# Kernel optimization log

Hardware: AMD Instinct MI355X
Metric: run time of the kernel (lower is better)

The kernel has to match this reference:

```python
import jax, jax.numpy as jnp
import numpy as np

NR, NA = 2, 1                 # num_raw, num_angle
QDIM = NR + 2 * NA            # 4: [r, x1=cos(th), x2=sin(th)]
DQ = NR + NA                  # 3: [dr, dth]
D = 2 * NR + 3 * NA           # 7: full state dim
HID = 256
EPS = 1e-6


def setup_inputs() -> dict:
    key = jax.random.key(0)
    ks = jax.random.split(key, 4)
    B = 32768
    x = jax.random.normal(ks[0], (B, D), dtype=jnp.float32)
    W0 = jax.random.normal(ks[1], (HID, D), dtype=jnp.float32) / np.sqrt(D)
    b0 = jnp.zeros((HID,), dtype=jnp.float32)
    W1 = jax.random.normal(ks[2], (HID, HID), dtype=jnp.float32) / np.sqrt(HID)
    b1 = jnp.zeros((HID,), dtype=jnp.float32)
    W2 = jax.random.normal(ks[3], (1, HID), dtype=jnp.float32) / np.sqrt(HID)
    b2 = jnp.zeros((1,), dtype=jnp.float32)
    return {"x": x, "W0": W0, "b0": b0, "W1": W1, "b1": b1, "W2": W2, "b2": b2}


def _lnn_forward(x, W0, b0, W1, b1, W2, b2):
    def L_single(xi):  # scalar Lagrangian of one state (D,)
        h = jnp.tanh(W0 @ xi + b0)
        h = jnp.tanh(W1 @ h + b1)
        return (W2 @ h + b2)[0]

    grad_single = jax.grad(L_single)
    gradL = jax.vmap(grad_single)(x)                       # (B, D)

    # Rows of the Hessian corresponding to d/d(dr,dth): (B, DQ, D).
    # Replaces the torch per-row autograd.grad loop with one batched jacfwd.
    def g(xi):
        return grad_single(xi)[QDIM:]                      # dL/d(dr,dth), (DQ,)
    Hrows = jax.vmap(jax.jacfwd(g))(x)                     # (B, DQ, D)

    x1 = x[:, NR:NR + NA]                                  # cos part (B, NA)
    x2 = x[:, NR + NA:QDIM]                                # sin part (B, NA)

    Jr = Hrows[:, :, :NR]                                  # (B, DQ, NR)
    Jx1 = Hrows[:, :, NR:NR + NA]                          # (B, DQ, NA)
    Jx2 = Hrows[:, :, NR + NA:QDIM]                        # (B, DQ, NA)
    Hdq = Hrows[:, :, QDIM:] + EPS * jnp.eye(DQ, dtype=x.dtype)  # (B, DQ, DQ)

    # chain rule back to angle theta: d/dth = -x2 * d/dx1 + x1 * d/dx2
    Jth = -x2[:, None, :] * Jx1 + x1[:, None, :] * Jx2     # (B, DQ, NA)
    Jrth = jnp.concatenate([Jr, Jth], axis=2)              # (B, DQ, DQ)

    dLdr = gradL[:, :NR]
    dLdx1 = gradL[:, NR:NR + NA]
    dLdx2 = gradL[:, NR + NA:QDIM]
    dLdth = -x2 * dLdx1 + x1 * dLdx2
    dLdrdth = jnp.concatenate([dLdr, dLdth], axis=1)       # (B, DQ)

    dq = x[:, QDIM:]                                       # (B, DQ)
    dq_term = jnp.einsum('bij,bj->bi', Jrth, dq)

    rhs = dLdrdth - dq_term                                # control = 0 (no controlNet)
    ddq = jnp.linalg.solve(Hdq, rhs[..., None])[..., 0]    # (B, DQ)

    dr = dq[:, :NR]
    dth = dq[:, NR:]
    dx1 = -x2 * dth
    dx2 = x1 * dth
    return jnp.concatenate([dr, dx1, dx2, ddq], axis=1)    # (B, D)


def reference(x, W0, b0, W1, b1, W2, b2):
    return _lnn_forward(x, W0, b0, W1, b1, W2, b2)
```

## Files before the change

### kernel.cpp

```cpp
#include <hip/hip_runtime.h>
#include <math.h>

#define HID 256
#define EPS_REG 1e-6

typedef __attribute__((ext_vector_type(8))) short short8;
typedef __attribute__((ext_vector_type(4))) short short4v;
typedef __attribute__((ext_vector_type(4))) float v4f;

#define MFMA_BF16(a, b, c) __builtin_amdgcn_mfma_f32_16x16x32_bf16((a), (b), (c), 0, 0, 0)

__device__ __forceinline__ float fast_tanh(float z) {
    const float e = __expf(2.0f * z);
    const float d = e + 1.0f;
    float r = __builtin_amdgcn_rcpf(d);
    r = r * (2.0f - d * r);
    return fmaf(-2.0f, r, 1.0f);
}

__device__ __forceinline__ float rtn_bf16(float v, short* s) {
    unsigned r = (__float_as_uint(v) + 0x8000u) & 0xFFFF0000u;
    *s = (short)(r >> 16);
    return __uint_as_float(r);
}
__device__ __forceinline__ void split3(float v, short* a, short* b, short* c) {
    float f0 = rtn_bf16(v, a);
    float r1 = v - f0;
    float f1 = rtn_bf16(r1, b);
    float r2 = r1 - f1;
    (void)rtn_bf16(r2, c);
}

__global__ void prep_w1_frags(const float* __restrict__ W1, short* __restrict__ ws) {
    const int gid   = blockIdx.x * 128 + threadIdx.x;
    const int lane  = gid & 63;
    const int ks    = (gid >> 6) & 7;
    const int rt    = (gid >> 9) & 15;
    const int which = gid >> 13;
    const int m = lane & 15, q = lane >> 4;

    float v[8];
    if (which == 0) {
        const float* p = W1 + (size_t)(rt*16 + m)*HID + ks*32 + q*8;
        const float4 va = *(const float4*)(p);
        const float4 vb = *(const float4*)(p + 4);
        v[0]=va.x; v[1]=va.y; v[2]=va.z; v[3]=va.w;
        v[4]=vb.x; v[5]=vb.y; v[6]=vb.z; v[7]=vb.w;
    } else {
        const float* p = W1 + (size_t)(ks*32 + q*8)*HID + rt*16 + m;
#pragma unroll
        for (int t = 0; t < 8; ++t) v[t] = p[(size_t)t*HID];
    }
    short8 h8, m8, l8;
#pragma unroll
    for (int t = 0; t < 8; ++t) {
        short sh, sm, sl;
        split3(v[t], &sh, &sm, &sl);
        h8[t] = sh; m8[t] = sm; l8[t] = sl;
    }
    const size_t base = (size_t)which*3*65536 + ((size_t)(rt*8 + ks)*64 + lane)*8;
    *(short8*)(ws + base)          = h8;
    *(short8*)(ws + base + 65536)  = m8;
    *(short8*)(ws + base + 131072) = l8;
}

#define FRAG_NT_STRIDE 13056
#define FRAG_BUF_STRIDE 4352

__device__ __forceinline__ void lnn_phase0(const float* __restrict__ x,
    const float* __restrict__ W0, const float* __restrict__ b0,
    int samp_base, short* __restrict__ Bf, float* __restrict__ M0, int tid)
{
    const int jq = tid & 63;
    const int s  = tid >> 6;
    const int j0 = jq * 4;
    const float* xs = x + (size_t)(samp_base + s)*7;
    float xv[7];
#pragma unroll
    for (int d = 0; d < 7; ++d) xv[d] = xs[d];
    float4 wv[7];
    const float* wp = W0 + (size_t)j0*7;
#pragma unroll
    for (int k = 0; k < 7; ++k) wv[k] = *(const float4*)(wp + 4*k);
    const float* wf = (const float*)wv;
    const int nt = s >> 2;
    const int cb = (s & 3) * 4;
    const int G  = j0 >> 3;
    const int t0 = j0 & 7;
    short4v hi4[4], mi4[4], lo4[4];
#pragma unroll
    for (int jj = 0; jj < 4; ++jj) {
        const int j = j0 + jj;
        float z = b0[j];
#pragma unroll
        for (int d = 0; d < 7; ++d) z = fmaf(wf[jj*7 + d], xv[d], z);
        const float h  = fast_tanh(z);
        const float sg = 1.0f - h*h;
        M0[j*9 + s] = h;
        float vals[4] = {h, sg*wf[jj*7 + 4], sg*wf[jj*7 + 5], sg*wf[jj*7 + 6]};
#pragma unroll
        for (int comp = 0; comp < 4; ++comp) {
            short sh, sm, sl;
            split3(vals[comp], &sh, &sm, &sl);
            hi4[comp][jj] = sh; mi4[comp][jj] = sm; lo4[comp][jj] = sl;
        }
    }
#pragma unroll
    for (int comp = 0; comp < 4; ++comp) {
        const int a = nt*FRAG_NT_STRIDE + G*136 + t0 + (cb + comp)*8;
        *(short4v*)(&Bf[a])                     = hi4[comp];
        *(short4v*)(&Bf[a + FRAG_BUF_STRIDE])   = mi4[comp];
        *(short4v*)(&Bf[a + 2*FRAG_BUF_STRIDE]) = lo4[comp];
    }
}

__device__ __forceinline__ void lnn_mm(const short8* __restrict__ Ah,
    const short8* __restrict__ Am, const short8* __restrict__ Al,
    const short* __restrict__ Bf, int w, int lane, int boff, v4f acc[2][2])
{
    short8 pah[2][2], pam[2][2], pal[2][2];
#pragma unroll
    for (int rtl = 0; rtl < 2; ++rtl) {
        const size_t fi = ((size_t)((w*2 + rtl)*8))*64 + lane;
        pah[0][rtl] = Ah[fi]; pam[0][rtl] = Am[fi]; pal[0][rtl] = Al[fi];
    }
#pragma unroll
    for (int ks = 0; ks < 8; ++ks) {
        const int cur = ks & 1, nxt = cur ^ 1;
        if (ks < 7) {
#pragma unroll
            for (int rtl = 0; rtl < 2; ++rtl) {
                const size_t fi = ((size_t)((w*2 + rtl)*8 + ks + 1))*64 + lane;
                pah[nxt][rtl] = Ah[fi]; pam[nxt][rtl] = Am[fi]; pal[nxt][rtl] = Al[fi];
            }
        }
        short8 bh[2], bm[2], bl[2];
#pragma unroll
        for (int nt = 0; nt < 2; ++nt) {
            const int a = nt*FRAG_NT_STRIDE + ks*544 + boff;
            bh[nt] = *(const short8*)(&Bf[a]);
            bm[nt] = *(const short8*)(&Bf[a + FRAG_BUF_STRIDE]);
            bl[nt] = *(const short8*)(&Bf[a + 2*FRAG_BUF_STRIDE]);
        }
        const short8 ah0 = pah[cur][0], ah1 = pah[cur][1];
        const short8 am0 = pam[cur][0], am1 = pam[cur][1];
        const short8 al0 = pal[cur][0], al1 = pal[cur][1];
        acc[0][0] = MFMA_BF16(ah0, bl[0], acc[0][0]);
        acc[0][1] = MFMA_BF16(ah0, bl[1], acc[0][1]);
        acc[1][0] = MFMA_BF16(ah1, bl[0], acc[1][0]);
        acc[1][1] = MFMA_BF16(ah1, bl[1], acc[1][1]);

        acc[0][0] = MFMA_BF16(al0, bh[0], acc[0][0]);
        acc[0][1] = MFMA_BF16(al0, bh[1], acc[0][1]);
        acc[1][0] = MFMA_BF16(al1, bh[0], acc[1][0]);
        acc[1][1] = MFMA_BF16(al1, bh[1], acc[1][1]);

        acc[0][0] = MFMA_BF16(am0, bm[0], acc[0][0]);
        acc[0][1] = MFMA_BF16(am0, bm[1], acc[0][1]);
        acc[1][0] = MFMA_BF16(am1, bm[0], acc[1][0]);
        acc[1][1] = MFMA_BF16(am1, bm[1], acc[1][1]);

        acc[0][0] = MFMA_BF16(am0, bh[0], acc[0][0]);
        acc[0][1] = MFMA_BF16(am0, bh[1], acc[0][1]);
        acc[1][0] = MFMA_BF16(am1, bh[0], acc[1][0]);
        acc[1][1] = MFMA_BF16(am1, bh[1], acc[1][1]);

        acc[0][0] = MFMA_BF16(ah0, bm[0], acc[0][0]);
        acc[0][1] = MFMA_BF16(ah0, bm[1], acc[0][1]);
        acc[1][0] = MFMA_BF16(ah1, bm[0], acc[1][0]);
        acc[1][1] = MFMA_BF16(ah1, bm[1], acc[1][1]);

        acc[0][0] = MFMA_BF16(ah0, bh[0], acc[0][0]);
        acc[0][1] = MFMA_BF16(ah0, bh[1], acc[0][1]);
        acc[1][0] = MFMA_BF16(ah1, bh[0], acc[1][0]);
        acc[1][1] = MFMA_BF16(ah1, bh[1], acc[1][1]);
    }
}

__device__ __forceinline__ void lnn_epi1(v4f acc[2][2], short* __restrict__ Bf,
    const float* __restrict__ b1, const float* __restrict__ W2,
    int w, int lane, int q, int c)
{
    const int myreg = c & 3;
    const int qbase = lane & ~3;
#pragma unroll
    for (int rtl = 0; rtl < 2; ++rtl) {
        const int base = (w*2 + rtl)*16;
        float b1r[4], w2r[4];
#pragma unroll
        for (int r = 0; r < 4; ++r) {
            b1r[r] = b1[base + q*4 + r];
            w2r[r] = W2[base + q*4 + r];
        }
        const int G  = (base >> 3) + (q >> 1);
        const int tq = (q & 1) * 4;
#pragma unroll
        for (int nt = 0; nt < 2; ++nt) {
            const float zb0 = __shfl(acc[rtl][nt][0] + b1r[0], qbase, 64);
            const float zb1 = __shfl(acc[rtl][nt][1] + b1r[1], qbase, 64);
            const float zb2 = __shfl(acc[rtl][nt][2] + b1r[2], qbase, 64);
            const float zb3 = __shfl(acc[rtl][nt][3] + b1r[3], qbase, 64);
            const float zsel = (myreg == 0) ? zb0
                             : (myreg == 1) ? zb1
                             : (myreg == 2) ? zb2 : zb3;
            const float ht = fast_tanh(zsel);
            const float st = 1.0f - ht*ht;
            float h1v[4], s1v[4];
#pragma unroll
            for (int r = 0; r < 4; ++r) {
                h1v[r] = __shfl(ht, qbase + r, 64);
                s1v[r] = __shfl(st, qbase + r, 64);
            }
            short4v ph, pm, pl;
#pragma unroll
            for (int r = 0; r < 4; ++r) {
                const float av = acc[rtl][nt][r];
                const float u  = (myreg == 0) ? (w2r[r]*s1v[r])
                                              : (-2.0f*w2r[r]*h1v[r]*s1v[r])*av;
                short sh, sm, sl;
                split3(u, &sh, &sm, &sl);
                ph[r] = sh; pm[r] = sm; pl[r] = sl;
            }
            const int a = nt*FRAG_NT_STRIDE + G*136 + c*8 + tq;
            *(short4v*)(&Bf[a])                     = ph;
            *(short4v*)(&Bf[a + FRAG_BUF_STRIDE])   = pm;
            *(short4v*)(&Bf[a + 2*FRAG_BUF_STRIDE]) = pl;
        }
    }
}

__device__ __forceinline__ void lnn_epi2(v4f acc2[2][2], short* __restrict__ Bf,
    const float* __restrict__ M0, const float* __restrict__ W0,
    int w, int lane, int q, int c)
{
    float* U0 = (float*)Bf;
#pragma unroll
    for (int rtl = 0; rtl < 2; ++rtl) {
#pragma unroll
        for (int reg = 0; reg < 4; ++reg) {
            const int j = (w*2 + rtl)*16 + q*4 + reg;
            const float w0sel = W0[j*7 + 3 + (c & 3)];
#pragma unroll
            for (int nt = 0; nt < 2; ++nt) {
                const int s = nt*4 + (c >> 2);
                const float pv = acc2[rtl][nt][reg];
                const float p0 = __shfl(pv, lane & ~3, 64);
                const float h0 = M0[j*9 + s];
                const float sg = 1.0f - h0*h0;
                const float t2 = -2.0f * p0 * h0 * sg;
                const float res = ((c & 3) == 0) ? (p0*sg)
                                                 : fmaf(pv, sg, t2 * w0sel);
                U0[j*36 + s*4 + (c & 3)] = res;
            }
        }
    }
}

__device__ __forceinline__ void lnn_phase3(const float* __restrict__ x,
    const float* __restrict__ W0, short* __restrict__ Bf,
    int samp_base, float* __restrict__ out, int w, int tid)
{
    const float* U0 = (const float*)Bf;
    float* scratch = ((float*)Bf) + 9216 + w * 425;
    const int t = tid & 63;
    float part[25];
#pragma unroll
    for (int qq = 0; qq < 25; ++qq) part[qq] = 0.0f;

#pragma unroll
    for (int m = 0; m < 4; ++m) {
        const int j = t + 64*m;
        const float4 uv = *(const float4*)(&U0[j*36 + w*4]);
        float w0d[7];
#pragma unroll
        for (int d = 0; d < 7; ++d) w0d[d] = W0[j*7 + d];
#pragma unroll
        for (int d = 0; d < 4; ++d) part[d] = fmaf(uv.x, w0d[d], part[d]);
#pragma unroll
        for (int d = 0; d < 7; ++d) {
            part[4  + d] = fmaf(uv.y, w0d[d], part[4  + d]);
            part[11 + d] = fmaf(uv.z, w0d[d], part[11 + d]);
            part[18 + d] = fmaf(uv.w, w0d[d], part[18 + d]);
        }
    }
#pragma unroll
    for (int off = 1; off <= 2; off <<= 1)
#pragma unroll
        for (int qq = 0; qq < 25; ++qq)
            part[qq] += __shfl_xor(part[qq], off, 64);
    {
        const int quad = t >> 2;
        if ((t & 3) == 0) {
#pragma unroll
            for (int e = 0; e < 25; ++e)
                scratch[e*17 + quad] = part[e];
        }
    }
    if (t < 25) {
        float tot = 0.0f;
#pragma unroll
        for (int k = 0; k < 16; ++k) tot += scratch[t*17 + k];
        scratch[t*17 + 16] = tot;
    }

    if (t == 0) {
        double g[25];
#pragma unroll
        for (int e = 0; e < 25; ++e) g[e] = (double)scratch[e*17 + 16];

        const float* xs = x + (size_t)(samp_base + w)*7;
        const double x1 = xs[2], x2 = xs[3];
        const double dq0 = xs[4], dq1 = xs[5], dth = xs[6];

        double M[3][3], rhs[3];
#pragma unroll
        for (int i = 0; i < 3; ++i) {
            const double J0 = g[4 + i*7 + 0];
            const double J1 = g[4 + i*7 + 1];
            const double J2 = -x2*g[4 + i*7 + 2] + x1*g[4 + i*7 + 3];
            const double dL = (i == 0) ? g[0]
                            : (i == 1) ? g[1]
                            : (-x2*g[2] + x1*g[3]);
            M[i][0] = g[4 + i*7 + 4] + (i == 0 ? EPS_REG : 0.0);
            M[i][1] = g[4 + i*7 + 5] + (i == 1 ? EPS_REG : 0.0);
            M[i][2] = g[4 + i*7 + 6] + (i == 2 ? EPS_REG : 0.0);
            rhs[i]  = dL - (J0*dq0 + J1*dq1 + J2*dth);
        }
        const double c00 = M[1][1]*M[2][2] - M[1][2]*M[2][1];
        const double c01 = M[1][2]*M[2][0] - M[1][0]*M[2][2];
        const double c02 = M[1][0]*M[2][1] - M[1][1]*M[2][0];
        const double det = M[0][0]*c00 + M[0][1]*c01 + M[0][2]*c02;
        const double inv = 1.0 / det;
        const double c10 = M[0][2]*M[2][1] - M[0][1]*M[2][2];
        const double c11 = M[0][0]*M[2][2] - M[0][2]*M[2][0];
        const double c12 = M[0][1]*M[2][0] - M[0][0]*M[2][1];
        const double c20 = M[0][1]*M[1][2] - M[0][2]*M[1][1];
        const double c21 = M[0][2]*M[1][0] - M[0][0]*M[1][2];
        const double c22 = M[0][0]*M[1][1] - M[0][1]*M[1][0];
        const double sol0 = (c00*rhs[0] + c10*rhs[1] + c20*rhs[2]) * inv;
        const double sol1 = (c01*rhs[0] + c11*rhs[1] + c21*rhs[2]) * inv;
        const double sol2 = (c02*rhs[0] + c12*rhs[1] + c22*rhs[2]) * inv;

        float* o = out + (size_t)(samp_base + w)*7;
        o[0] = (float)dq0;
        o[1] = (float)dq1;
        o[2] = (float)(-x2*dth);
        o[3] = (float)( x1*dth);
        o[4] = (float)sol0;
        o[5] = (float)sol1;
        o[6] = (float)sol2;
    }
}

__global__ __launch_bounds__(512, 4)
void lnn_mfma(const float* __restrict__ x,
              const float* __restrict__ W0, const float* __restrict__ b0,
              const float* __restrict__ b1, const float* __restrict__ W2,
              const short* __restrict__ ws,
              float* __restrict__ out)
{
    __shared__ __align__(16) short Bfrag[26112];
    __shared__ float M0h[HID * 9];

    const int tid   = threadIdx.x;
    const int samp0 = blockIdx.x * 8;
    const int lane  = tid & 63;
    const int w     = tid >> 6;

    lnn_phase0(x, W0, b0, samp0, Bfrag, M0h, tid);
    __syncthreads();

    const short8* A1h = (const short8*)ws;
    const short8* A1m = A1h + 8192;
    const short8* A1l = A1h + 16384;
    const short8* A2h = A1h + 24576;
    const short8* A2m = A1h + 32768;
    const short8* A2l = A1h + 40960;

    const int q = lane >> 4;
    const int c = lane & 15;
    const int boff = q*136 + c*8;

    v4f acc[2][2];
#pragma unroll
    for (int r = 0; r < 2; ++r)
#pragma unroll
        for (int n = 0; n < 2; ++n) acc[r][n] = (v4f){0.f, 0.f, 0.f, 0.f};
    lnn_mm(A1h, A1m, A1l, Bfrag, w, lane, boff, acc);
    __syncthreads();

    lnn_epi1(acc, Bfrag, b1, W2, w, lane, q, c);
    __syncthreads();

    v4f acc2[2][2];
#pragma unroll
    for (int r = 0; r < 2; ++r)
#pragma unroll
        for (int n = 0; n < 2; ++n) acc2[r][n] = (v4f){0.f, 0.f, 0.f, 0.f};
    lnn_mm(A2h, A2m, A2l, Bfrag, w, lane, boff, acc2);
    __syncthreads();

    lnn_epi2(acc2, Bfrag, M0h, W0, w, lane, q, c);
    __syncthreads();

    lnn_phase3(x, W0, Bfrag, samp0, out, w, tid);
}

#define TS8 8
#define SCP 36

__global__ void transpose_w1(const float* __restrict__ W1, float* __restrict__ W1T) {
    __shared__ float tile[32][33];
    const int bx = blockIdx.x & 7;
    const int by = blockIdx.x >> 3;
    const int tx = threadIdx.x & 31;
    const int ty = threadIdx.x >> 5;
#pragma unroll
    for (int q = 0; q < 4; ++q)
        tile[ty + q*8][tx] = W1[(by*32 + ty + q*8)*HID + bx*32 + tx];
    __syncthreads();
#pragma unroll
    for (int q = 0; q < 4; ++q)
        W1T[(bx*32 + ty + q*8)*HID + by*32 + tx] = tile[tx][ty + q*8];
}

__global__ __launch_bounds__(256, 2)
void lnn_fused(const float* __restrict__ x,
               const float* __restrict__ W0, const float* __restrict__ b0,
               const float* __restrict__ W1, const float* __restrict__ b1,
               const float* __restrict__ W2,
               const float* __restrict__ W1T, const int useT,
               float* __restrict__ out)
{
    __shared__ float M0[HID * SCP];
    __shared__ float U [HID * SCP];
    const int tid   = threadIdx.x;
    const int samp0 = blockIdx.x * TS8;
    {
        const int j = tid;
        float w0r[7];
#pragma unroll
        for (int d = 0; d < 7; ++d) w0r[d] = W0[j*7 + d];
        const float bj = b0[j];
#pragma unroll
        for (int s = 0; s < TS8; ++s) {
            const float* xs = x + (size_t)(samp0 + s)*7;
            float z = bj;
#pragma unroll
            for (int d = 0; d < 7; ++d) z = fmaf(w0r[d], xs[d], z);
            const float h  = tanhf(z);
            const float sg = 1.0f - h*h;
            float4 v = {h, sg * w0r[4], sg * w0r[5], sg * w0r[6]};
            *(float4*)(&M0[j*SCP + s*4]) = v;
        }
    }
    __syncthreads();
    const int it = tid & 63;
    const int ct = tid >> 6;
    float acc[4][8];
#pragma unroll
    for (int r = 0; r < 4; ++r)
#pragma unroll
        for (int c = 0; c < 8; ++c) acc[r][c] = 0.0f;
    if (useT) {
#pragma unroll 4
        for (int j = 0; j < HID; ++j) {
            const float4 w4 = *(const float4*)(W1T + (size_t)j*HID + it*4);
            const float4 ma = *(const float4*)(&M0[j*SCP + ct*8]);
            const float4 mb = *(const float4*)(&M0[j*SCP + ct*8 + 4]);
            const float w[4] = {w4.x, w4.y, w4.z, w4.w};
            const float m[8] = {ma.x, ma.y, ma.z, ma.w, mb.x, mb.y, mb.z, mb.w};
#pragma unroll
            for (int r = 0; r < 4; ++r)
#pragma unroll
                for (int c = 0; c < 8; ++c)
                    acc[r][c] = fmaf(w[r], m[c], acc[r][c]);
        }
    } else {
#pragma unroll 2
        for (int j = 0; j < HID; ++j) {
            float w[4];
#pragma unroll
            for (int r = 0; r < 4; ++r) w[r] = W1[(size_t)(it*4 + r)*HID + j];
            const float4 ma = *(const float4*)(&M0[j*SCP + ct*8]);
            const float4 mb = *(const float4*)(&M0[j*SCP + ct*8 + 4]);
            const float m[8] = {ma.x, ma.y, ma.z, ma.w, mb.x, mb.y, mb.z, mb.w};
#pragma unroll
            for (int r = 0; r < 4; ++r)
#pragma unroll
                for (int c = 0; c < 8; ++c)
                    acc[r][c] = fmaf(w[r], m[c], acc[r][c]);
        }
    }
    {
#pragma unroll
        for (int r = 0; r < 4; ++r) {
            const int i = it*4 + r;
            const float b1i = b1[i];
            const float w2i = W2[i];
#pragma unroll
            for (int cs = 0; cs < 2; ++cs) {
                const float z1 = acc[r][cs*4+0] + b1i;
                const float h1 = tanhf(z1);
                const float s1 = 1.0f - h1*h1;
                float4 uv;
                uv.x = w2i * s1;
                const float m2 = -2.0f * w2i * h1 * s1;
                uv.y = m2 * acc[r][cs*4+1];
                uv.z = m2 * acc[r][cs*4+2];
                uv.w = m2 * acc[r][cs*4+3];
                *(float4*)(&U[i*SCP + ct*8 + cs*4]) = uv;
            }
        }
    }
    __syncthreads();
    float acc2[4][8];
#pragma unroll
    for (int r = 0; r < 4; ++r)
#pragma unroll
        for (int c = 0; c < 8; ++c) acc2[r][c] = 0.0f;
#pragma unroll 4
    for (int i = 0; i < HID; ++i) {
        const float4 w4 = *(const float4*)(W1 + (size_t)i*HID + it*4);
        const float4 ua = *(const float4*)(&U[i*SCP + ct*8]);
        const float4 ub = *(const float4*)(&U[i*SCP + ct*8 + 4]);
        const float w[4] = {w4.x, w4.y, w4.z, w4.w};
        const float m[8] = {ua.x, ua.y, ua.z, ua.w, ub.x, ub.y, ub.z, ub.w};
#pragma unroll
        for (int r = 0; r < 4; ++r)
#pragma unroll
            for (int c = 0; c < 8; ++c)
                acc2[r][c] = fmaf(w[r], m[c], acc2[r][c]);
    }
    __syncthreads();
    {
#pragma unroll
        for (int r = 0; r < 4; ++r) {
            const int j = it*4 + r;
#pragma unroll
            for (int cs = 0; cs < 2; ++cs) {
                const int scb = ct*8 + cs*4;
                const float4 mm = *(const float4*)(&M0[j*SCP + scb]);
                const float h0v = mm.x;
                const float sg  = 1.0f - h0v*h0v;
                const float p   = acc2[r][cs*4+0];
                const float t2  = -2.0f * p * h0v;
                float4 uv;
                uv.x = p * sg;
                uv.y = fmaf(acc2[r][cs*4+1], sg, t2 * mm.y);
                uv.z = fmaf(acc2[r][cs*4+2], sg, t2 * mm.z);
                uv.w = fmaf(acc2[r][cs*4+3], sg, t2 * mm.w);
                *(float4*)(&U[j*SCP + scb]) = uv;
            }
        }
    }
    __syncthreads();
    const int s = tid >> 5;
    const int t = tid & 31;
    float part[25];
#pragma unroll
    for (int qq = 0; qq < 25; ++qq) part[qq] = 0.0f;
#pragma unroll
    for (int m = 0; m < 8; ++m) {
        const int j = t + 32*m;
        const float4 uv = *(const float4*)(&U[j*SCP + s*4]);
        float w0d[7];
#pragma unroll
        for (int d = 0; d < 7; ++d) w0d[d] = W0[j*7 + d];
#pragma unroll
        for (int d = 0; d < 4; ++d) part[d] = fmaf(uv.x, w0d[d], part[d]);
#pragma unroll
        for (int d = 0; d < 7; ++d) {
            part[4  + d] = fmaf(uv.y, w0d[d], part[4  + d]);
            part[11 + d] = fmaf(uv.z, w0d[d], part[11 + d]);
            part[18 + d] = fmaf(uv.w, w0d[d], part[18 + d]);
        }
    }
#pragma unroll
    for (int off = 16; off >= 1; off >>= 1)
#pragma unroll
        for (int qq = 0; qq < 25; ++qq)
            part[qq] += __shfl_xor(part[qq], off, 64);
    if (t == 0) {
        const float* xs = x + (size_t)(samp0 + s)*7;
        const double x1 = xs[2], x2 = xs[3];
        const double dq0 = xs[4], dq1 = xs[5], dth = xs[6];
        double A[3][4];
#pragma unroll
        for (int i = 0; i < 3; ++i) {
            const double J0 = part[4 + i*7 + 0];
            const double J1 = part[4 + i*7 + 1];
            const double J2 = -x2*(double)part[4 + i*7 + 2] + x1*(double)part[4 + i*7 + 3];
            const double dL = (i == 0) ? (double)part[0]
                            : (i == 1) ? (double)part[1]
                            : (-x2*(double)part[2] + x1*(double)part[3]);
            A[i][0] = (double)part[4 + i*7 + 4] + (i == 0 ? EPS_REG : 0.0);
            A[i][1] = (double)part[4 + i*7 + 5] + (i == 1 ? EPS_REG : 0.0);
            A[i][2] = (double)part[4 + i*7 + 6] + (i == 2 ? EPS_REG : 0.0);
            A[i][3] = dL - (J0*dq0 + J1*dq1 + J2*dth);
        }
        for (int cc = 0; cc < 2; ++cc) {
            int piv = cc;
            double mx = fabs(A[cc][cc]);
            for (int rr = cc + 1; rr < 3; ++rr) {
                const double v = fabs(A[rr][cc]);
                if (v > mx) { mx = v; piv = rr; }
            }
            if (piv != cc) {
                for (int k2 = 0; k2 < 4; ++k2) {
                    const double tmp = A[cc][k2]; A[cc][k2] = A[piv][k2]; A[piv][k2] = tmp;
                }
            }
            const double inv = 1.0 / A[cc][cc];
            for (int rr = cc + 1; rr < 3; ++rr) {
                const double f = A[rr][cc] * inv;
                for (int k2 = cc + 1; k2 < 4; ++k2) A[rr][k2] -= f * A[cc][k2];
            }
        }
        const double sol2 = A[2][3] / A[2][2];
        const double sol1 = (A[1][3] - A[1][2]*sol2) / A[1][1];
        const double sol0 = (A[0][3] - A[0][1]*sol1 - A[0][2]*sol2) / A[0][0];
        float* o = out + (size_t)(samp0 + s)*7;
        o[0] = (float)dq0;
        o[1] = (float)dq1;
        o[2] = (float)(-x2*dth);
        o[3] = (float)( x1*dth);
        o[4] = (float)sol0;
        o[5] = (float)sol1;
        o[6] = (float)sol2;
    }
}

extern "C" void kernel_launch(void* const* d_in, const int* in_sizes, int n_in,
                              void* d_out, int out_size, void* d_ws, size_t ws_size,
                              hipStream_t stream) {
    const float* x  = (const float*)d_in[0];
    const float* W0 = (const float*)d_in[1];
    const float* b0 = (const float*)d_in[2];
    const float* W1 = (const float*)d_in[3];
    const float* b1 = (const float*)d_in[4];
    const float* W2 = (const float*)d_in[5];
    float* out = (float*)d_out;

    const int B = in_sizes[0] / 7;
    const size_t NEED = 6u * 65536u * sizeof(short);

    if (ws_size >= NEED && (B % 8) == 0) {
        short* ws = (short*)d_ws;
        prep_w1_frags<<<128, 128, 0, stream>>>(W1, ws);
        lnn_mfma<<<B / 8, 512, 0, stream>>>(x, W0, b0, b1, W2, ws, out);
    } else {
        const int useT = (ws_size >= (size_t)HID * HID * sizeof(float)) ? 1 : 0;
        float* W1T = (float*)d_ws;
        if (useT) transpose_w1<<<64, 256, 0, stream>>>(W1, W1T);
        lnn_fused<<<B / TS8, 256, 0, stream>>>(x, W0, b0, W1, b1, W2, W1T, useT, out);
    }
}
```

Measured before the change: 276.0 us.

## Switch W1 matmuls to 32x32x16 bf16 MFMA with re-laid-out fragments

Replaces the 16x16x32 bf16 MFMA tiling (2x2 accumulator tiles per wave) with a single 32x32x16 MFMA accumulator per wave. The W1 fragment prep, the phase-0 B-fragment construction (now using cross-lane shuffles), and both epilogues are rewritten for the new register layout. The final 3x3 solve moves to a separate step where 8 threads each handle one sample after a barrier. The intent is fewer MFMA issues and less LDS fragment traffic per K step, at the cost of more shuffles in phase 0 and an extra synchronization.

```diff
diff --git a/kernel.cpp b/kernel.cpp
--- a/kernel.cpp
+++ b/kernel.cpp
@@ -4,11 +4,11 @@
 #define HID 256
 #define EPS_REG 1e-6
 
-typedef __attribute__((ext_vector_type(8))) short short8;
-typedef __attribute__((ext_vector_type(4))) short short4v;
-typedef __attribute__((ext_vector_type(4))) float v4f;
-
-#define MFMA_BF16(a, b, c) __builtin_amdgcn_mfma_f32_16x16x32_bf16((a), (b), (c), 0, 0, 0)
+typedef __attribute__((ext_vector_type(8)))  short short8;
+typedef __attribute__((ext_vector_type(4)))  short short4v;
+typedef __attribute__((ext_vector_type(16))) float v16f;
+
+#define MFMA32(a, b, c) __builtin_amdgcn_mfma_f32_32x32x16_bf16((a), (b), (c), 0, 0, 0)
 
 __device__ __forceinline__ float fast_tanh(float z) {
     const float e = __expf(2.0f * z);
@@ -34,20 +34,21 @@
 __global__ void prep_w1_frags(const float* __restrict__ W1, short* __restrict__ ws) {
     const int gid   = blockIdx.x * 128 + threadIdx.x;
     const int lane  = gid & 63;
-    const int ks    = (gid >> 6) & 7;
-    const int rt    = (gid >> 9) & 15;
+    const int kstep = (gid >> 6) & 15;
+    const int rt    = (gid >> 10) & 7;
     const int which = gid >> 13;
-    const int m = lane & 15, q = lane >> 4;
+    const int r32   = lane & 31;
+    const int kh    = lane >> 5;
 
     float v[8];
     if (which == 0) {
-        const float* p = W1 + (size_t)(rt*16 + m)*HID + ks*32 + q*8;
+        const float* p = W1 + (size_t)(rt*32 + r32)*HID + kstep*16 + kh*8;
         const float4 va = *(const float4*)(p);
         const float4 vb = *(const float4*)(p + 4);
         v[0]=va.x; v[1]=va.y; v[2]=va.z; v[3]=va.w;
         v[4]=vb.x; v[5]=vb.y; v[6]=vb.z; v[7]=vb.w;
     } else {
-        const float* p = W1 + (size_t)(ks*32 + q*8)*HID + rt*16 + m;
+        const float* p = W1 + (size_t)(kstep*16 + kh*8)*HID + rt*32 + r32;
 #pragma unroll
         for (int t = 0; t < 8; ++t) v[t] = p[(size_t)t*HID];
     }
@@ -58,207 +59,162 @@
         split3(v[t], &sh, &sm, &sl);
         h8[t] = sh; m8[t] = sm; l8[t] = sl;
     }
-    const size_t base = (size_t)which*3*65536 + ((size_t)(rt*8 + ks)*64 + lane)*8;
+    const size_t base = (size_t)which*196608 + ((size_t)(rt*16 + kstep)*64 + lane)*8;
     *(short8*)(ws + base)          = h8;
     *(short8*)(ws + base + 65536)  = m8;
     *(short8*)(ws + base + 131072) = l8;
 }
 
-#define FRAG_NT_STRIDE 13056
-#define FRAG_BUF_STRIDE 4352
+#define SMEM_SHORTS 25248
 
 __device__ __forceinline__ void lnn_phase0(const float* __restrict__ x,
     const float* __restrict__ W0, const float* __restrict__ b0,
     int samp_base, short* __restrict__ Bf, float* __restrict__ M0, int tid)
 {
-    const int jq = tid & 63;
-    const int s  = tid >> 6;
-    const int j0 = jq * 4;
+    const int col  = tid & 31;
+    const int s    = col >> 2;
+    const int comp = col & 3;
+    const int grp  = tid >> 5;
+    const int jb   = grp * 16;
+    const int lane = tid & 63;
+
     const float* xs = x + (size_t)(samp_base + s)*7;
     float xv[7];
 #pragma unroll
     for (int d = 0; d < 7; ++d) xv[d] = xs[d];
-    float4 wv[7];
-    const float* wp = W0 + (size_t)j0*7;
-#pragma unroll
-    for (int k = 0; k < 7; ++k) wv[k] = *(const float4*)(wp + 4*k);
-    const float* wf = (const float*)wv;
-    const int nt = s >> 2;
-    const int cb = (s & 3) * 4;
-    const int G  = j0 >> 3;
-    const int t0 = j0 & 7;
-    short4v hi4[4], mi4[4], lo4[4];
+
+    float hown[4];
 #pragma unroll
     for (int jj = 0; jj < 4; ++jj) {
-        const int j = j0 + jj;
+        const int j = jb + comp*4 + jj;
         float z = b0[j];
 #pragma unroll
-        for (int d = 0; d < 7; ++d) z = fmaf(wf[jj*7 + d], xv[d], z);
-        const float h  = fast_tanh(z);
-        const float sg = 1.0f - h*h;
-        M0[j*9 + s] = h;
-        float vals[4] = {h, sg*wf[jj*7 + 4], sg*wf[jj*7 + 5], sg*wf[jj*7 + 6]};
-#pragma unroll
-        for (int comp = 0; comp < 4; ++comp) {
+        for (int d = 0; d < 7; ++d) z = fmaf(W0[j*7 + d], xv[d], z);
+        hown[jj] = fast_tanh(z);
+        M0[j*9 + s] = hown[jj];
+    }
+
+#pragma unroll
+    for (int oct = 0; oct < 2; ++oct) {
+        short8 vh, vm, vl;
+#pragma unroll
+        for (int k = 0; k < 8; ++k) {
+            const int jidx = oct*8 + k;
+            const int j = jb + jidx;
+            const int owner = (lane & ~3) | (jidx >> 2);
+            float hsrc;
+            switch (jidx & 3) {
+                case 0: hsrc = hown[0]; break;
+                case 1: hsrc = hown[1]; break;
+                case 2: hsrc = hown[2]; break;
+                default: hsrc = hown[3]; break;
+            }
+            const float h  = __shfl(hsrc, owner, 64);
+            const float sg = 1.0f - h*h;
+            const float val = (comp == 0) ? h : (sg * W0[j*7 + 3 + comp]);
             short sh, sm, sl;
-            split3(vals[comp], &sh, &sm, &sl);
-            hi4[comp][jj] = sh; mi4[comp][jj] = sm; lo4[comp][jj] = sl;
-        }
-    }
-#pragma unroll
-    for (int comp = 0; comp < 4; ++comp) {
-        const int a = nt*FRAG_NT_STRIDE + G*136 + t0 + (cb + comp)*8;
-        *(short4v*)(&Bf[a])                     = hi4[comp];
-        *(short4v*)(&Bf[a + FRAG_BUF_STRIDE])   = mi4[comp];
-        *(short4v*)(&Bf[a + 2*FRAG_BUF_STRIDE]) = lo4[comp];
-    }
-}
-
-__device__ __forceinline__ void lnn_mm(const short8* __restrict__ Ah,
+            split3(val, &sh, &sm, &sl);
+            vh[k] = sh; vm[k] = sm; vl[k] = sl;
+        }
+        const int o = grp*2 + oct;
+        const int a = (o*32 + col)*8;
+        *(short8*)(&Bf[a])         = vh;
+        *(short8*)(&Bf[a + 8192])  = vm;
+        *(short8*)(&Bf[a + 16384]) = vl;
+    }
+}
+
+__device__ __forceinline__ void lnn_mm32(const short8* __restrict__ Ah,
     const short8* __restrict__ Am, const short8* __restrict__ Al,
-    const short* __restrict__ Bf, int w, int lane, int boff, v4f acc[2][2])
-{
-    short8 pah[2][2], pam[2][2], pal[2][2];
-#pragma unroll
-    for (int rtl = 0; rtl < 2; ++rtl) {
-        const size_t fi = ((size_t)((w*2 + rtl)*8))*64 + lane;
-        pah[0][rtl] = Ah[fi]; pam[0][rtl] = Am[fi]; pal[0][rtl] = Al[fi];
-    }
-#pragma unroll
-    for (int ks = 0; ks < 8; ++ks) {
+    const short* __restrict__ Bf, int w, int lane, v16f& acc)
+{
+    short8 pah[2], pam[2], pal[2];
+    {
+        const size_t fi = ((size_t)(w*16))*64 + lane;
+        pah[0] = Ah[fi]; pam[0] = Am[fi]; pal[0] = Al[fi];
+    }
+#pragma unroll
+    for (int ks = 0; ks < 16; ++ks) {
         const int cur = ks & 1, nxt = cur ^ 1;
-        if (ks < 7) {
-#pragma unroll
-            for (int rtl = 0; rtl < 2; ++rtl) {
-                const size_t fi = ((size_t)((w*2 + rtl)*8 + ks + 1))*64 + lane;
-                pah[nxt][rtl] = Ah[fi]; pam[nxt][rtl] = Am[fi]; pal[nxt][rtl] = Al[fi];
-            }
-        }
-        short8 bh[2], bm[2], bl[2];
-#pragma unroll
-        for (int nt = 0; nt < 2; ++nt) {
-            const int a = nt*FRAG_NT_STRIDE + ks*544 + boff;
-            bh[nt] = *(const short8*)(&Bf[a]);
-            bm[nt] = *(const short8*)(&Bf[a + FRAG_BUF_STRIDE]);
-            bl[nt] = *(const short8*)(&Bf[a + 2*FRAG_BUF_STRIDE]);
-        }
-        const short8 ah0 = pah[cur][0], ah1 = pah[cur][1];
-        const short8 am0 = pam[cur][0], am1 = pam[cur][1];
-        const short8 al0 = pal[cur][0], al1 = pal[cur][1];
-        acc[0][0] = MFMA_BF16(ah0, bl[0], acc[0][0]);
-        acc[0][1] = MFMA_BF16(ah0, bl[1], acc[0][1]);
-        acc[1][0] = MFMA_BF16(ah1, bl[0], acc[1][0]);
-        acc[1][1] = MFMA_BF16(ah1, bl[1], acc[1][1]);
-
-        acc[0][0] = MFMA_BF16(al0, bh[0], acc[0][0]);
-        acc[0][1] = MFMA_BF16(al0, bh[1], acc[0][1]);
-        acc[1][0] = MFMA_BF16(al1, bh[0], acc[1][0]);
-        acc[1][1] = MFMA_BF16(al1, bh[1], acc[1][1]);
-
-        acc[0][0] = MFMA_BF16(am0, bm[0], acc[0][0]);
-        acc[0][1] = MFMA_BF16(am0, bm[1], acc[0][1]);
-        acc[1][0] = MFMA_BF16(am1, bm[0], acc[1][0]);
-        acc[1][1] = MFMA_BF16(am1, bm[1], acc[1][1]);
-
-        acc[0][0] = MFMA_BF16(am0, bh[0], acc[0][0]);
-        acc[0][1] = MFMA_BF16(am0, bh[1], acc[0][1]);
-        acc[1][0] = MFMA_BF16(am1, bh[0], acc[1][0]);
-        acc[1][1] = MFMA_BF16(am1, bh[1], acc[1][1]);
-
-        acc[0][0] = MFMA_BF16(ah0, bm[0], acc[0][0]);
-        acc[0][1] = MFMA_BF16(ah0, bm[1], acc[0][1]);
-        acc[1][0] = MFMA_BF16(ah1, bm[0], acc[1][0]);
-        acc[1][1] = MFMA_BF16(ah1, bm[1], acc[1][1]);
-
-        acc[0][0] = MFMA_BF16(ah0, bh[0], acc[0][0]);
-        acc[0][1] = MFMA_BF16(ah0, bh[1], acc[0][1]);
-        acc[1][0] = MFMA_BF16(ah1, bh[0], acc[1][0]);
-        acc[1][1] = MFMA_BF16(ah1, bh[1], acc[1][1]);
-    }
-}
-
-__device__ __forceinline__ void lnn_epi1(v4f acc[2][2], short* __restrict__ Bf,
-    const float* __restrict__ b1, const float* __restrict__ W2,
-    int w, int lane, int q, int c)
-{
-    const int myreg = c & 3;
-    const int qbase = lane & ~3;
-#pragma unroll
-    for (int rtl = 0; rtl < 2; ++rtl) {
-        const int base = (w*2 + rtl)*16;
-        float b1r[4], w2r[4];
-#pragma unroll
-        for (int r = 0; r < 4; ++r) {
-            b1r[r] = b1[base + q*4 + r];
-            w2r[r] = W2[base + q*4 + r];
-        }
-        const int G  = (base >> 3) + (q >> 1);
-        const int tq = (q & 1) * 4;
-#pragma unroll
-        for (int nt = 0; nt < 2; ++nt) {
-            const float zb0 = __shfl(acc[rtl][nt][0] + b1r[0], qbase, 64);
-            const float zb1 = __shfl(acc[rtl][nt][1] + b1r[1], qbase, 64);
-            const float zb2 = __shfl(acc[rtl][nt][2] + b1r[2], qbase, 64);
-            const float zb3 = __shfl(acc[rtl][nt][3] + b1r[3], qbase, 64);
-            const float zsel = (myreg == 0) ? zb0
-                             : (myreg == 1) ? zb1
-                             : (myreg == 2) ? zb2 : zb3;
-            const float ht = fast_tanh(zsel);
-            const float st = 1.0f - ht*ht;
-            float h1v[4], s1v[4];
-#pragma unroll
-            for (int r = 0; r < 4; ++r) {
-                h1v[r] = __shfl(ht, qbase + r, 64);
-                s1v[r] = __shfl(st, qbase + r, 64);
-            }
-            short4v ph, pm, pl;
-#pragma unroll
-            for (int r = 0; r < 4; ++r) {
-                const float av = acc[rtl][nt][r];
-                const float u  = (myreg == 0) ? (w2r[r]*s1v[r])
-                                              : (-2.0f*w2r[r]*h1v[r]*s1v[r])*av;
-                short sh, sm, sl;
-                split3(u, &sh, &sm, &sl);
-                ph[r] = sh; pm[r] = sm; pl[r] = sl;
-            }
-            const int a = nt*FRAG_NT_STRIDE + G*136 + c*8 + tq;
-            *(short4v*)(&Bf[a])                     = ph;
-            *(short4v*)(&Bf[a + FRAG_BUF_STRIDE])   = pm;
-            *(short4v*)(&Bf[a + 2*FRAG_BUF_STRIDE]) = pl;
-        }
-    }
-}
-
-__device__ __forceinline__ void lnn_epi2(v4f acc2[2][2], short* __restrict__ Bf,
-    const float* __restrict__ M0, const float* __restrict__ W0,
-    int w, int lane, int q, int c)
+        if (ks < 15) {
+            const size_t fi = ((size_t)(w*16 + ks + 1))*64 + lane;
+            pah[nxt] = Ah[fi]; pam[nxt] = Am[fi]; pal[nxt] = Al[fi];
+        }
+        const int a = (ks*64 + lane)*8;
+        const short8 bh = *(const short8*)(&Bf[a]);
+        const short8 bm = *(const short8*)(&Bf[a + 8192]);
+        const short8 bl = *(const short8*)(&Bf[a + 16384]);
+        const short8 ah = pah[cur], am = pam[cur], al = pal[cur];
+        acc = MFMA32(ah, bl, acc);
+        acc = MFMA32(al, bh, acc);
+        acc = MFMA32(am, bm, acc);
+        acc = MFMA32(am, bh, acc);
+        acc = MFMA32(ah, bm, acc);
+        acc = MFMA32(ah, bh, acc);
+    }
+}
+
+__device__ __forceinline__ void lnn_epi1_32(const v16f& acc, short* __restrict__ Bf,
+    const float* __restrict__ b1, const float* __restrict__ W2, int w, int lane)
+{
+    const int col  = lane & 31;
+    const int comp = lane & 3;
+    const int hb   = lane >> 5;
+    const int ib   = w*32 + 4*hb;
+#pragma unroll
+    for (int rg = 0; rg < 4; ++rg) {
+        short4v ph, pm, pl;
+#pragma unroll
+        for (int rr = 0; rr < 4; ++rr) {
+            const int reg = rg*4 + rr;
+            const int i = ib + 8*rg + rr;
+            const float z0 = __shfl(acc[reg] + b1[i], lane & ~3, 64);
+            const float h1 = fast_tanh(z0);
+            const float s1 = 1.0f - h1*h1;
+            const float av = acc[reg];
+            const float w2i = W2[i];
+            const float u  = (comp == 0) ? (w2i*s1)
+                                         : (-2.0f*w2i*h1*s1)*av;
+            short sh, sm, sl;
+            split3(u, &sh, &sm, &sl);
+            ph[rr] = sh; pm[rr] = sm; pl[rr] = sl;
+        }
+        const int a = (((w*2 + (rg>>1))*64) + (((rg & 1) << 5) | col))*8 + 4*hb;
+        *(short4v*)(&Bf[a])         = ph;
+        *(short4v*)(&Bf[a + 8192])  = pm;
+        *(short4v*)(&Bf[a + 16384]) = pl;
+    }
+}
+
+__device__ __forceinline__ void lnn_epi2_32(const v16f& acc2, short* __restrict__ Bf,
+    const float* __restrict__ M0, const float* __restrict__ W0, int w, int lane)
 {
     float* U0 = (float*)Bf;
-#pragma unroll
-    for (int rtl = 0; rtl < 2; ++rtl) {
-#pragma unroll
-        for (int reg = 0; reg < 4; ++reg) {
-            const int j = (w*2 + rtl)*16 + q*4 + reg;
-            const float w0sel = W0[j*7 + 3 + (c & 3)];
-#pragma unroll
-            for (int nt = 0; nt < 2; ++nt) {
-                const int s = nt*4 + (c >> 2);
-                const float pv = acc2[rtl][nt][reg];
-                const float p0 = __shfl(pv, lane & ~3, 64);
-                const float h0 = M0[j*9 + s];
-                const float sg = 1.0f - h0*h0;
-                const float t2 = -2.0f * p0 * h0 * sg;
-                const float res = ((c & 3) == 0) ? (p0*sg)
-                                                 : fmaf(pv, sg, t2 * w0sel);
-                U0[j*36 + s*4 + (c & 3)] = res;
-            }
-        }
-    }
-}
-
-__device__ __forceinline__ void lnn_phase3(const float* __restrict__ x,
-    const float* __restrict__ W0, short* __restrict__ Bf,
-    int samp_base, float* __restrict__ out, int w, int tid)
+    const int col  = lane & 31;
+    const int s    = col >> 2;
+    const int comp = lane & 3;
+    const int hb   = lane >> 5;
+#pragma unroll
+    for (int rg = 0; rg < 4; ++rg) {
+#pragma unroll
+        for (int rr = 0; rr < 4; ++rr) {
+            const int reg = rg*4 + rr;
+            const int j = w*32 + 8*rg + 4*hb + rr;
+            const float w0sel = W0[j*7 + 3 + comp];
+            const float pv = acc2[reg];
+            const float p0 = __shfl(pv, lane & ~3, 64);
+            const float h0 = M0[j*9 + s];
+            const float sg = 1.0f - h0*h0;
+            const float t2 = -2.0f * p0 * h0 * sg;
+            const float res = (comp == 0) ? (p0*sg)
+                                          : fmaf(pv, sg, t2 * w0sel);
+            U0[j*36 + col] = res;
+        }
+    }
+}
+
+__device__ __forceinline__ void lnn_phase3_sums(const float* __restrict__ W0,
+    short* __restrict__ Bf, int w, int tid)
 {
     const float* U0 = (const float*)Bf;
     float* scratch = ((float*)Bf) + 9216 + w * 425;
@@ -302,64 +258,69 @@
         for (int k = 0; k < 16; ++k) tot += scratch[t*17 + k];
         scratch[t*17 + 16] = tot;
     }
-
-    if (t == 0) {
-        double g[25];
-#pragma unroll
-        for (int e = 0; e < 25; ++e) g[e] = (double)scratch[e*17 + 16];
-
-        const float* xs = x + (size_t)(samp_base + w)*7;
-        const double x1 = xs[2], x2 = xs[3];
-        const double dq0 = xs[4], dq1 = xs[5], dth = xs[6];
-
-        double M[3][3], rhs[3];
-#pragma unroll
-        for (int i = 0; i < 3; ++i) {
-            const double J0 = g[4 + i*7 + 0];
-            const double J1 = g[4 + i*7 + 1];
-            const double J2 = -x2*g[4 + i*7 + 2] + x1*g[4 + i*7 + 3];
-            const double dL = (i == 0) ? g[0]
-                            : (i == 1) ? g[1]
-                            : (-x2*g[2] + x1*g[3]);
-            M[i][0] = g[4 + i*7 + 4] + (i == 0 ? EPS_REG : 0.0);
-            M[i][1] = g[4 + i*7 + 5] + (i == 1 ? EPS_REG : 0.0);
-            M[i][2] = g[4 + i*7 + 6] + (i == 2 ? EPS_REG : 0.0);
-            rhs[i]  = dL - (J0*dq0 + J1*dq1 + J2*dth);
-        }
-        const double c00 = M[1][1]*M[2][2] - M[1][2]*M[2][1];
-        const double c01 = M[1][2]*M[2][0] - M[1][0]*M[2][2];
-        const double c02 = M[1][0]*M[2][1] - M[1][1]*M[2][0];
-        const double det = M[0][0]*c00 + M[0][1]*c01 + M[0][2]*c02;
-        const double inv = 1.0 / det;
-        const double c10 = M[0][2]*M[2][1] - M[0][1]*M[2][2];
-        const double c11 = M[0][0]*M[2][2] - M[0][2]*M[2][0];
-        const double c12 = M[0][1]*M[2][0] - M[0][0]*M[2][1];
-        const double c20 = M[0][1]*M[1][2] - M[0][2]*M[1][1];
-        const double c21 = M[0][2]*M[1][0] - M[0][0]*M[1][2];
-        const double c22 = M[0][0]*M[1][1] - M[0][1]*M[1][0];
-        const double sol0 = (c00*rhs[0] + c10*rhs[1] + c20*rhs[2]) * inv;
-        const double sol1 = (c01*rhs[0] + c11*rhs[1] + c21*rhs[2]) * inv;
-        const double sol2 = (c02*rhs[0] + c12*rhs[1] + c22*rhs[2]) * inv;
-
-        float* o = out + (size_t)(samp_base + w)*7;
-        o[0] = (float)dq0;
-        o[1] = (float)dq1;
-        o[2] = (float)(-x2*dth);
-        o[3] = (float)( x1*dth);
-        o[4] = (float)sol0;
-        o[5] = (float)sol1;
-        o[6] = (float)sol2;
-    }
+}
+
+__device__ __forceinline__ void lnn_solve8(const float* __restrict__ x,
+    short* __restrict__ Bf, int samp_base, float* __restrict__ out, int tid)
+{
+    if (tid >= 8) return;
+    const int s = tid;
+    const float* scratch = ((const float*)Bf) + 9216 + s * 425;
+    double g[25];
+#pragma unroll
+    for (int e = 0; e < 25; ++e) g[e] = (double)scratch[e*17 + 16];
+
+    const float* xs = x + (size_t)(samp_base + s)*7;
+    const double x1 = xs[2], x2 = xs[3];
+    const double dq0 = xs[4], dq1 = xs[5], dth = xs[6];
+
+    double M[3][3], rhs[3];
+#pragma unroll
+    for (int i = 0; i < 3; ++i) {
+        const double J0 = g[4 + i*7 + 0];
+        const double J1 = g[4 + i*7 + 1];
+        const double J2 = -x2*g[4 + i*7 + 2] + x1*g[4 + i*7 + 3];
+        const double dL = (i == 0) ? g[0]
+                        : (i == 1) ? g[1]
+                        : (-x2*g[2] + x1*g[3]);
+        M[i][0] = g[4 + i*7 + 4] + (i == 0 ? EPS_REG : 0.0);
+        M[i][1] = g[4 + i*7 + 5] + (i == 1 ? EPS_REG : 0.0);
+        M[i][2] = g[4 + i*7 + 6] + (i == 2 ? EPS_REG : 0.0);
+        rhs[i]  = dL - (J0*dq0 + J1*dq1 + J2*dth);
+    }
+    const double c00 = M[1][1]*M[2][2] - M[1][2]*M[2][1];
+    const double c01 = M[1][2]*M[2][0] - M[1][0]*M[2][2];
+    const double c02 = M[1][0]*M[2][1] - M[1][1]*M[2][0];
+    const double det = M[0][0]*c00 + M[0][1]*c01 + M[0][2]*c02;
+    const double inv = 1.0 / det;
+    const double c10 = M[0][2]*M[2][1] - M[0][1]*M[2][2];
+    const double c11 = M[0][0]*M[2][2] - M[0][2]*M[2][0];
+    const double c12 = M[0][1]*M[2][0] - M[0][0]*M[2][1];
+    const double c20 = M[0][1]*M[1][2] - M[0][2]*M[1][1];
+    const double c21 = M[0][2]*M[1][0] - M[0][0]*M[1][2];
+    const double c22 = M[0][0]*M[1][1] - M[0][1]*M[1][0];
+    const double sol0 = (c00*rhs[0] + c10*rhs[1] + c20*rhs[2]) * inv;
+    const double sol1 = (c01*rhs[0] + c11*rhs[1] + c21*rhs[2]) * inv;
+    const double sol2 = (c02*rhs[0] + c12*rhs[1] + c22*rhs[2]) * inv;
+
+    float* o = out + (size_t)(samp_base + s)*7;
+    o[0] = (float)dq0;
+    o[1] = (float)dq1;
+    o[2] = (float)(-x2*dth);
+    o[3] = (float)( x1*dth);
+    o[4] = (float)sol0;
+    o[5] = (float)sol1;
+    o[6] = (float)sol2;
 }
 
 __global__ __launch_bounds__(512, 4)
-void lnn_mfma(const float* __restrict__ x,
-              const float* __restrict__ W0, const float* __restrict__ b0,
-              const float* __restrict__ b1, const float* __restrict__ W2,
-              const short* __restrict__ ws,
-              float* __restrict__ out)
-{
-    __shared__ __align__(16) short Bfrag[26112];
+void lnn_mfma32(const float* __restrict__ x,
+                const float* __restrict__ W0, const float* __restrict__ b0,
+                const float* __restrict__ b1, const float* __restrict__ W2,
+                const short* __restrict__ ws,
+                float* __restrict__ out)
+{
+    __shared__ __align__(16) short Bfrag[SMEM_SHORTS];
     __shared__ float M0h[HID * 9];
 
     const int tid   = threadIdx.x;
@@ -377,33 +338,28 @@
     const short8* A2m = A1h + 32768;
     const short8* A2l = A1h + 40960;
 
-    const int q = lane >> 4;
-    const int c = lane & 15;
-    const int boff = q*136 + c*8;
-
-    v4f acc[2][2];
-#pragma unroll
-    for (int r = 0; r < 2; ++r)
-#pragma unroll
-        for (int n = 0; n < 2; ++n) acc[r][n] = (v4f){0.f, 0.f, 0.f, 0.f};
-    lnn_mm(A1h, A1m, A1l, Bfrag, w, lane, boff, acc);
-    __syncthreads();
-
-    lnn_epi1(acc, Bfrag, b1, W2, w, lane, q, c);
-    __syncthreads();
-
-    v4f acc2[2][2];
-#pragma unroll
-    for (int r = 0; r < 2; ++r)
-#pragma unroll
-        for (int n = 0; n < 2; ++n) acc2[r][n] = (v4f){0.f, 0.f, 0.f, 0.f};
-    lnn_mm(A2h, A2m, A2l, Bfrag, w, lane, boff, acc2);
-    __syncthreads();
-
-    lnn_epi2(acc2, Bfrag, M0h, W0, w, lane, q, c);
-    __syncthreads();
-
-    lnn_phase3(x, W0, Bfrag, samp0, out, w, tid);
+    v16f acc;
+#pragma unroll
+    for (int i = 0; i < 16; ++i) acc[i] = 0.0f;
+    lnn_mm32(A1h, A1m, A1l, Bfrag, w, lane, acc);
+    __syncthreads();
+
+    lnn_epi1_32(acc, Bfrag, b1, W2, w, lane);
+    __syncthreads();
+
+    v16f acc2;
+#pragma unroll
+    for (int i = 0; i < 16; ++i) acc2[i] = 0.0f;
+    lnn_mm32(A2h, A2m, A2l, Bfrag, w, lane, acc2);
+    __syncthreads();
+
+    lnn_epi2_32(acc2, Bfrag, M0h, W0, w, lane);
+    __syncthreads();
+
+    lnn_phase3_sums(W0, Bfrag, w, tid);
+    __syncthreads();
+
+    lnn_solve8(x, Bfrag, samp0, out, tid);
 }
 
 #define TS8 8
@@ -648,7 +604,7 @@
     if (ws_size >= NEED && (B % 8) == 0) {
         short* ws = (short*)d_ws;
         prep_w1_frags<<<128, 128, 0, stream>>>(W1, ws);
-        lnn_mfma<<<B / 8, 512, 0, stream>>>(x, W0, b0, b1, W2, ws, out);
+        lnn_mfma32<<<B / 8, 512, 0, stream>>>(x, W0, b0, b1, W2, ws, out);
     } else {
         const int useT = (ws_size >= (size_t)HID * HID * sizeof(float)) ? 1 : 0;
         float* W1T = (float*)d_ws;
```

After: 295.4 us. +7.0%, slower.
